# Performance work log

Hardware: AMD Instinct MI355X
Metric: run time of the kernel (lower is better)

## Reference

```python
import jax, jax.numpy as jnp
import numpy as np

VOCAB = 32000
HID = 1024
CUTOFFS = [0, 10000, 20000, 32000]
N_CLUSTERS = 2
DIV = 4
PROJ_DIMS = [HID // DIV**i for i in range(N_CLUSTERS + 1)]  # [1024, 256, 64]
# Faithful to source quirk: n_vocabs = cutoffs[i] + cutoffs[i+1]
LOGIT_DIMS = [CUTOFFS[i] + CUTOFFS[i + 1] for i in range(N_CLUSTERS + 1)]  # [10000, 30000, 52000]


def setup_inputs() -> dict:
    key = jax.random.key(0)
    ks = jax.random.split(key, 16)
    N = 2048
    inp = {
        "x": jax.random.normal(ks[0], (N, HID), dtype=jnp.float32),
        "y": jax.random.randint(ks[1], (N,), 0, VOCAB, dtype=jnp.int64),
    }
    s = 0.02
    # projections: Linear(hidden, proj_dims[i], bias=False); stored as [in, out]
    inp["Wp0"] = jax.random.normal(ks[2], (HID, PROJ_DIMS[0]), dtype=jnp.float32) * s
    inp["Wp1"] = jax.random.normal(ks[3], (HID, PROJ_DIMS[1]), dtype=jnp.float32) * s
    inp["Wp2"] = jax.random.normal(ks[4], (HID, PROJ_DIMS[2]), dtype=jnp.float32) * s
    # logits: Linear(proj_dims[i], LOGIT_DIMS[i]) with bias
    inp["Wl0"] = jax.random.normal(ks[5], (PROJ_DIMS[0], LOGIT_DIMS[0]), dtype=jnp.float32) * s
    inp["bl0"] = jnp.zeros((LOGIT_DIMS[0],), dtype=jnp.float32)
    inp["Wl1"] = jax.random.normal(ks[6], (PROJ_DIMS[1], LOGIT_DIMS[1]), dtype=jnp.float32) * s
    inp["bl1"] = jnp.zeros((LOGIT_DIMS[1],), dtype=jnp.float32)
    inp["Wl2"] = jax.random.normal(ks[7], (PROJ_DIMS[2], LOGIT_DIMS[2]), dtype=jnp.float32) * s
    inp["bl2"] = jnp.zeros((LOGIT_DIMS[2],), dtype=jnp.float32)
    # cluster_logit: Linear(hidden, n_clusters)
    inp["Wc"] = jax.random.normal(ks[8], (HID, N_CLUSTERS), dtype=jnp.float32) * s
    inp["bc"] = jnp.zeros((N_CLUSTERS,), dtype=jnp.float32)
    return inp


def reference(x, y, Wp0, Wp1, Wp2, Wl0, bl0, Wl1, bl1, Wl2, bl2, Wc, bc):
    # head: project (dim-preserving here) then head-vocab logits + cluster logits
    head_proj = x @ Wp0                                   # [N, 1024]
    head_logit = jnp.concatenate(
        [head_proj @ Wl0 + bl0, head_proj @ Wc + bc], axis=1
    )                                                     # [N, 10000 + 2]
    head_lp = jax.nn.log_softmax(head_logit, axis=1)

    nll = jnp.zeros(y.shape, dtype=x.dtype)

    # cluster 0: targets in [0, cutoffs[1])
    m0 = (y >= CUTOFFS[0]) & (y < CUTOFFS[1])
    t0 = jnp.clip(y - CUTOFFS[0], 0, head_lp.shape[1] - 1)
    lp0 = jnp.take_along_axis(head_lp, t0[:, None], axis=1)[:, 0]
    nll = jnp.where(m0, -lp0, nll)

    # tail clusters: small projection GEMM + log_softmax + gather, combined via masks
    tails = [(Wp1, Wl1, bl1), (Wp2, Wl2, bl2)]
    for i, (Wp, Wl, bl) in enumerate(tails, start=1):
        l, r = CUTOFFS[i], CUTOFFS[i + 1]
        mask = (y >= l) & (y < r)
        t = jnp.clip(y - l, 0, Wl.shape[1] - 1)
        tail_lp = jax.nn.log_softmax((x @ Wp) @ Wl + bl, axis=1)  # [N, LOGIT_DIMS[i]]
        # faithful to source: head column -i (reversed cluster order quirk)
        lp = head_lp[:, -i] + jnp.take_along_axis(tail_lp, t[:, None], axis=1)[:, 0]
        nll = jnp.where(mask, -lp, nll)

    return nll
```

## Files before the change

### kernel.cpp

```cpp
#include <hip/hip_runtime.h>
#include <math.h>

#define HID 1024
#define NROWS 2048

typedef __attribute__((ext_vector_type(8))) short short8;
typedef __attribute__((ext_vector_type(4))) short short4_t;
typedef __attribute__((ext_vector_type(4))) float f32x4;

__device__ __forceinline__ short f2bf(float f) {
  union { float f; unsigned u; } v; v.f = f;
  unsigned r = v.u + 0x7fffu + ((v.u >> 16) & 1u);
  return (short)(r >> 16);
}
__device__ __forceinline__ float bf2f(short s) {
  union { unsigned u; float f; } v; v.u = ((unsigned)(unsigned short)s) << 16;
  return v.f;
}
__device__ __forceinline__ float wave_sum(float a) {
#pragma unroll
  for (int off = 32; off; off >>= 1) a += __shfl_xor(a, off, 64);
  return a;
}

__global__ __launch_bounds__(256) void prep(
    const float* __restrict__ x, const int* __restrict__ y,
    const float* __restrict__ Wp0, const float* __restrict__ Wp1,
    const float* __restrict__ Wp2, const float* __restrict__ Wl0,
    const float* __restrict__ Wl1, const float* __restrict__ Wl2,
    short* __restrict__ xb,
    int* __restrict__ counts, int* __restrict__ slot_of_row,
    int* __restrict__ rows1, int* __restrict__ rows2,
    short* __restrict__ T0, short* __restrict__ T1, short* __restrict__ T2,
    short* __restrict__ T3, short* __restrict__ T4, short* __restrict__ T5) {
  const int tid = threadIdx.x;
  int b = blockIdx.x;
  if (b == 0) {
    __shared__ int c1s, c2s;
    if (tid == 0) { c1s = 0; c2s = 0; }
    __syncthreads();
    for (int r = tid; r < NROWS; r += 256) {
      const int yy = y[r];
      if (yy >= 20000) {
        const int s = atomicAdd(&c2s, 1);
        slot_of_row[r] = s; rows2[s] = r;
      } else if (yy >= 10000) {
        const int s = atomicAdd(&c1s, 1);
        slot_of_row[r] = s; rows1[s] = r;
      } else {
        slot_of_row[r] = -1;
      }
    }
    __syncthreads();
    if (tid == 0) { counts[0] = NROWS; counts[1] = c1s; counts[2] = c2s; }
    return;
  }
  if (b <= 2048) {
    const int i = ((b - 1) * 256 + tid) * 4;
    short4_t o;
    o.x = f2bf(x[i + 0]); o.y = f2bf(x[i + 1]);
    o.z = f2bf(x[i + 2]); o.w = f2bf(x[i + 3]);
    *(short4_t*)&xb[i] = o;
    return;
  }
  b -= 2049;
  const float* W; short* BT; int K, N, Npad, tn;
  if (b < 1024)                { W = Wp0; BT = T0; K = 1024; N = 1024;  Npad = 1024;  tn = 32;   }
  else if ((b -= 1024) < 256)  { W = Wp1; BT = T1; K = 1024; N = 256;   Npad = 256;   tn = 8;    }
  else if ((b -= 256) < 128)   { W = Wp2; BT = T2; K = 1024; N = 64;    Npad = 128;   tn = 4;    }
  else if ((b -= 128) < 10112) { W = Wl0; BT = T3; K = 1024; N = 10000; Npad = 10112; tn = 316;  }
  else if ((b -= 10112) < 7520){ W = Wl1; BT = T4; K = 256;  N = 30000; Npad = 30080; tn = 940;  }
  else { b -= 7520;              W = Wl2; BT = T5; K = 64;   N = 52000; Npad = 52096; tn = 1628; }

  __shared__ float T[32][33];
  const int n0 = (b % tn) * 32, k0 = (b / tn) * 32;
  const int r = tid >> 3, c = (tid & 7) * 4;
  float v0 = 0.f, v1 = 0.f, v2 = 0.f, v3 = 0.f;
  const float* p = &W[(size_t)(k0 + r) * N];
  if (n0 + c + 3 < N) {
    v0 = p[n0 + c]; v1 = p[n0 + c + 1]; v2 = p[n0 + c + 2]; v3 = p[n0 + c + 3];
  } else {
    if (n0 + c + 0 < N) v0 = p[n0 + c + 0];
    if (n0 + c + 1 < N) v1 = p[n0 + c + 1];
    if (n0 + c + 2 < N) v2 = p[n0 + c + 2];
  }
  T[r][c] = v0; T[r][c + 1] = v1; T[r][c + 2] = v2; T[r][c + 3] = v3;
  __syncthreads();
  const int nl = tid >> 3, kl = (tid & 7) * 4;
  const int n = n0 + nl;
  if (n < Npad) {
    short4_t o;
    o.x = (n < N) ? f2bf(T[kl + 0][nl]) : (short)0;
    o.y = (n < N) ? f2bf(T[kl + 1][nl]) : (short)0;
    o.z = (n < N) ? f2bf(T[kl + 2][nl]) : (short)0;
    o.w = (n < N) ? f2bf(T[kl + 3][nl]) : (short)0;
    *(short4_t*)&BT[(size_t)n * K + k0 + kl] = o;
  }
}

__device__ __forceinline__ void mfma_mainloop(const short* aB[4], const short* bB[4],
                                              short* As, short* Bs,
                                              f32x4 acc[4][4],
                                              int K, int w, int lane) {
  const int quad = lane >> 4, ln = lane & 15;
  const int wm = w >> 1, wn = w & 1;
  const int l7 = ln & 7;
  for (int kt = 0; kt < K; kt += 64) {
#pragma unroll
    for (int i = 0; i < 4; ++i) {
      const int row = w * 32 + i * 8;
      __builtin_amdgcn_global_load_lds(
          (const __attribute__((address_space(1))) void*)(aB[i] + kt),
          (__attribute__((address_space(3))) void*)(As + row * 64), 16, 0, 0);
      __builtin_amdgcn_global_load_lds(
          (const __attribute__((address_space(1))) void*)(bB[i] + kt),
          (__attribute__((address_space(3))) void*)(Bs + row * 64), 16, 0, 0);
    }
    __syncthreads();
#pragma unroll
    for (int ks = 0; ks < 2; ++ks) {
      const int kcs = ks * 4 + quad;
      short8 af[4], bfr[4];
#pragma unroll
      for (int mt = 0; mt < 4; ++mt) {
        const int row = wm * 64 + mt * 16 + ln;
        af[mt] = *(const short8*)(As + ((row * 8 + (kcs ^ l7)) << 3));
      }
#pragma unroll
      for (int nt = 0; nt < 4; ++nt) {
        const int rowb = wn * 64 + nt * 16 + ln;
        bfr[nt] = *(const short8*)(Bs + ((rowb * 8 + (kcs ^ l7)) << 3));
      }
#pragma unroll
      for (int mt = 0; mt < 4; ++mt)
#pragma unroll
        for (int nt = 0; nt < 4; ++nt)
          acc[mt][nt] = __builtin_amdgcn_mfma_f32_16x16x32_bf16(
              af[mt], bfr[nt], acc[mt][nt], 0, 0, 0);
    }
    __syncthreads();
  }
}


__global__ __launch_bounds__(256) void proj_all(
    const short* __restrict__ xb,
    const short* __restrict__ WpT0, const short* __restrict__ WpT1,
    const short* __restrict__ WpT2,
    short* __restrict__ P0b, short* __restrict__ P1c, short* __restrict__ P2c,
    const int* __restrict__ rows1, const int* __restrict__ rows2,
    const int* __restrict__ counts) {
  int b = blockIdx.x;
  const short* BT; short* C; int N, r0, c0, cnt;
  const int* rowlist = nullptr;
  if (b < 128) {
    BT = WpT0; C = P0b; N = 1024;
    c0 = (b & 7) * 128; r0 = (b >> 3) * 128; cnt = NROWS;
  } else if (b < 160) {
    b -= 128; BT = WpT1; C = P1c; N = 256;
    c0 = (b & 1) * 128; r0 = (b >> 1) * 128; rowlist = rows1; cnt = counts[1];
  } else {
    b -= 160; BT = WpT2; C = P2c; N = 64;
    c0 = 0; r0 = b * 128; rowlist = rows2; cnt = counts[2];
  }
  if (r0 >= cnt) return;

  __shared__ short As[128 * 64];
  __shared__ short Bs[128 * 64];
  const int tid = threadIdx.x;
  const int w = tid >> 6, lane = tid & 63;
  const int quad = lane >> 4, ln = lane & 15;
  const int wm = w >> 1, wn = w & 1;
  const int rsub = lane >> 3;
  const int kc = (lane & 7) ^ rsub;
  const int K = 1024;

  const short* aB[4]; const short* bB[4];
#pragma unroll
  for (int i = 0; i < 4; ++i) {
    const int sl = r0 + w * 32 + i * 8 + rsub;
    const int ar = rowlist ? rowlist[sl < cnt ? sl : cnt - 1] : sl;
    aB[i] = xb + (size_t)ar * K + kc * 8;
    bB[i] = BT + (size_t)(c0 + w * 32 + i * 8 + rsub) * K + kc * 8;
  }

  f32x4 acc[4][4];
  const f32x4 zero = {0.f, 0.f, 0.f, 0.f};
#pragma unroll
  for (int i = 0; i < 4; ++i)
#pragma unroll
    for (int j = 0; j < 4; ++j) acc[i][j] = zero;
  mfma_mainloop(aB, bB, As, Bs, acc, K, w, lane);
#pragma unroll
  for (int mt = 0; mt < 4; ++mt)
#pragma unroll
    for (int r = 0; r < 4; ++r) {
      const int grow = r0 + wm * 64 + mt * 16 + quad * 4 + r;
#pragma unroll
      for (int nt = 0; nt < 4; ++nt) {
        const int cg = c0 + wn * 64 + nt * 16 + ln;
        if (cg < N) C[(size_t)grow * N + cg] = f2bf(acc[mt][nt][r]);
      }
    }
}

#define HB  (16 * 79)
#define T1B (16 * 235)
#define T2B (16 * 407)

__global__ __launch_bounds__(256) void logit_all(
    const short* __restrict__ P0b, const short* __restrict__ WlT0,
    const float* __restrict__ bl0, float* __restrict__ psh,
    const short* __restrict__ P1c, const short* __restrict__ WlT1,
    const float* __restrict__ bl1, float* __restrict__ ps1,
    const short* __restrict__ P2c, const short* __restrict__ WlT2,
    const float* __restrict__ bl2, float* __restrict__ ps2,
    const int* __restrict__ counts) {
  int b = blockIdx.x;
  const short* A; const short* BT; const float* bias; float* ps;
  int K, Ncols, nsplit, rb, cs, cnt;
  if (b < HB) {
    A = P0b; BT = WlT0; bias = bl0; ps = psh;
    K = 1024; Ncols = 10000; nsplit = 79; rb = b / 79; cs = b % 79; cnt = NROWS;
  } else if ((b -= HB) < T1B) {
    A = P1c; BT = WlT1; bias = bl1; ps = ps1;
    K = 256; Ncols = 30000; nsplit = 235; rb = b / 235; cs = b % 235; cnt = counts[1];
  } else {
    b -= T1B;
    A = P2c; BT = WlT2; bias = bl2; ps = ps2;
    K = 64; Ncols = 52000; nsplit = 407; rb = b / 407; cs = b % 407; cnt = counts[2];
  }
  const int r0 = rb * 128, c0 = cs * 128;
  if (r0 >= cnt) return;

  __shared__ short As[128 * 64];
  __shared__ short Bs[128 * 64];
  __shared__ float psL[2][128];
  const int tid = threadIdx.x;
  const int w = tid >> 6, lane = tid & 63;
  const int quad = lane >> 4, ln = lane & 15;
  const int wm = w >> 1, wn = w & 1;
  const int rsub = lane >> 3;
  const int kc = (lane & 7) ^ rsub;

  const short* aB[4]; const short* bB[4];
#pragma unroll
  for (int i = 0; i < 4; ++i) {
    aB[i] = A + (size_t)(r0 + w * 32 + i * 8 + rsub) * K + kc * 8;
    bB[i] = BT + (size_t)(c0 + w * 32 + i * 8 + rsub) * K + kc * 8;
  }

  f32x4 acc[4][4];
  const f32x4 zero = {0.f, 0.f, 0.f, 0.f};
#pragma unroll
  for (int i = 0; i < 4; ++i)
#pragma unroll
    for (int j = 0; j < 4; ++j) acc[i][j] = zero;
  mfma_mainloop(aB, bB, As, Bs, acc, K, w, lane);

  float bv[4], vm[4];
#pragma unroll
  for (int nt = 0; nt < 4; ++nt) {
    const int cg = c0 + wn * 64 + nt * 16 + ln;
    vm[nt] = (cg < Ncols) ? 1.f : 0.f;
    bv[nt] = (cg < Ncols) ? bias[cg] : 0.f;
  }
#pragma unroll
  for (int mt = 0; mt < 4; ++mt)
#pragma unroll
    for (int r = 0; r < 4; ++r) {
      float s = 0.f;
#pragma unroll
      for (int nt = 0; nt < 4; ++nt)
        s += vm[nt] * __expf(acc[mt][nt][r] + bv[nt]);
#pragma unroll
      for (int off = 1; off < 16; off <<= 1) s += __shfl_xor(s, off, 64);
      if (ln == 0) psL[wn][wm * 64 + mt * 16 + quad * 4 + r] = s;
    }
  __syncthreads();
  if (tid < 128)
    ps[(size_t)(r0 + tid) * nsplit + cs] = psL[0][tid] + psL[1][tid];
}

__global__ __launch_bounds__(256) void finalize(
    const short* __restrict__ P0b, const short* __restrict__ P1c,
    const short* __restrict__ P2c,
    const short* __restrict__ WlT0, const float* __restrict__ bl0,
    const short* __restrict__ WlT1, const float* __restrict__ bl1,
    const short* __restrict__ WlT2, const float* __restrict__ bl2,
    const float* __restrict__ Wc, const float* __restrict__ bc,
    const int* __restrict__ y, const int* __restrict__ slot_of_row,
    const float* __restrict__ psh, const float* __restrict__ ps1,
    const float* __restrict__ ps2, float* __restrict__ out) {
  const int lane = threadIdx.x & 63;
  const int row = blockIdx.x * 4 + (threadIdx.x >> 6);

  float a0 = 0.f, a1 = 0.f;
  for (int k = lane; k < HID; k += 64) {
    const float p = bf2f(P0b[(size_t)row * HID + k]);
    a0 += p * Wc[2 * k];
    a1 += p * Wc[2 * k + 1];
  }
  a0 = wave_sum(a0);
  a1 = wave_sum(a1);
  const float cl0 = a0 + bc[0], cl1 = a1 + bc[1];

  float S = 0.f;
  for (int i = lane; i < 79; i += 64) S += psh[(size_t)row * 79 + i];
  S = wave_sum(S) + __expf(cl0) + __expf(cl1);
  const float lse = logf(S);

  const int yy = y[row];
  float nll;
  if (yy < 10000) {
    const short* pr = P0b + (size_t)row * 1024;
    const short* wr = WlT0 + (size_t)yy * 1024;
    float a = 0.f;
    for (int kk = lane * 4; kk < 1024; kk += 256) {
      const short4_t p = *(const short4_t*)(pr + kk);
      const short4_t wv = *(const short4_t*)(wr + kk);
      a += bf2f(p.x) * bf2f(wv.x) + bf2f(p.y) * bf2f(wv.y)
         + bf2f(p.z) * bf2f(wv.z) + bf2f(p.w) * bf2f(wv.w);
    }
    a = wave_sum(a);
    nll = -((a + bl0[yy]) - lse);
  } else if (yy < 20000) {
    const int t = yy - 10000;
    const int slot = slot_of_row[row];
    float S1 = 0.f;
    for (int i = lane; i < 235; i += 64) S1 += ps1[(size_t)slot * 235 + i];
    S1 = wave_sum(S1);
    const short* pr = P1c + (size_t)slot * 256;
    const short* wr = WlT1 + (size_t)t * 256;
    const int kk = lane * 4;
    const short4_t p = *(const short4_t*)(pr + kk);
    const short4_t wv = *(const short4_t*)(wr + kk);
    float a = bf2f(p.x) * bf2f(wv.x) + bf2f(p.y) * bf2f(wv.y)
            + bf2f(p.z) * bf2f(wv.z) + bf2f(p.w) * bf2f(wv.w);
    a = wave_sum(a);
    nll = -((cl1 - lse) + ((a + bl1[t]) - logf(S1)));
  } else {
    const int t = yy - 20000;
    const int slot = slot_of_row[row];
    float S2 = 0.f;
    for (int i = lane; i < 407; i += 64) S2 += ps2[(size_t)slot * 407 + i];
    S2 = wave_sum(S2);
    float a = 0.f;
    if (lane < 16) {
      const short* pr = P2c + (size_t)slot * 64;
      const short* wr = WlT2 + (size_t)t * 64;
      const int kk = lane * 4;
      const short4_t p = *(const short4_t*)(pr + kk);
      const short4_t wv = *(const short4_t*)(wr + kk);
      a = bf2f(p.x) * bf2f(wv.x) + bf2f(p.y) * bf2f(wv.y)
        + bf2f(p.z) * bf2f(wv.z) + bf2f(p.w) * bf2f(wv.w);
    }
    a = wave_sum(a);
    nll = -((cl0 - lse) + ((a + bl2[t]) - logf(S2)));
  }
  if (lane == 0) out[row] = nll;
}

extern "C" void kernel_launch(void* const* d_in, const int* in_sizes, int n_in,
                              void* d_out, int out_size, void* d_ws, size_t ws_size,
                              hipStream_t stream) {
  const float* x   = (const float*)d_in[0];
  const int*   y   = (const int*)d_in[1];
  const float* Wp0 = (const float*)d_in[2];
  const float* Wp1 = (const float*)d_in[3];
  const float* Wp2 = (const float*)d_in[4];
  const float* Wl0 = (const float*)d_in[5];
  const float* bl0 = (const float*)d_in[6];
  const float* Wl1 = (const float*)d_in[7];
  const float* bl1 = (const float*)d_in[8];
  const float* Wl2 = (const float*)d_in[9];
  const float* bl2 = (const float*)d_in[10];
  const float* Wc  = (const float*)d_in[11];
  const float* bc  = (const float*)d_in[12];
  float* out = (float*)d_out;

  float* fws = (float*)d_ws;
  float* psh = fws; fws += (size_t)NROWS * 79;
  float* ps1 = fws; fws += (size_t)NROWS * 235;
  float* ps2 = fws; fws += (size_t)NROWS * 407;
  int* iws = (int*)fws;
  int* counts      = iws; iws += 4;
  int* slot_of_row = iws; iws += NROWS;
  int* rows1       = iws; iws += NROWS;
  int* rows2       = iws; iws += NROWS;
  short* sp = (short*)iws;
  short* xb   = sp; sp += (size_t)NROWS * 1024;
  short* P0b  = sp; sp += (size_t)NROWS * 1024;
  short* P1c  = sp; sp += (size_t)NROWS * 256;
  short* P2c  = sp; sp += (size_t)NROWS * 64;
  short* WpT0 = sp; sp += (size_t)1024 * 1024;
  short* WpT1 = sp; sp += (size_t)256 * 1024;
  short* WpT2 = sp; sp += (size_t)128 * 1024;
  short* WlT0 = sp; sp += (size_t)10112 * 1024;
  short* WlT1 = sp; sp += (size_t)30080 * 256;
  short* WlT2 = sp; sp += (size_t)52096 * 64;

  dim3 blk(256);
  prep<<<dim3(24345), blk, 0, stream>>>(x, y, Wp0, Wp1, Wp2, Wl0, Wl1, Wl2,
                                        xb, counts, slot_of_row, rows1, rows2,
                                        WpT0, WpT1, WpT2, WlT0, WlT1, WlT2);
  proj_all<<<dim3(176), blk, 0, stream>>>(xb, WpT0, WpT1, WpT2, P0b, P1c, P2c,
                                          rows1, rows2, counts);
  logit_all<<<dim3(HB + T1B + T2B), blk, 0, stream>>>(
      P0b, WlT0, bl0, psh, P1c, WlT1, bl1, ps1, P2c, WlT2, bl2, ps2, counts);
  finalize<<<dim3(NROWS / 4), blk, 0, stream>>>(
      P0b, P1c, P2c, WlT0, bl0, WlT1, bl1, WlT2, bl2, Wc, bc, y, slot_of_row,
      psh, ps1, ps2, out);
}
```

Measured before the change: 318.9 us.

## Overlap logit weight transposes with projection GEMM; persistent XCD-aware logit kernel

```diff
diff --git a/kernel.cpp b/kernel.cpp
--- a/kernel.cpp
+++ b/kernel.cpp
@@ -23,16 +23,44 @@
   return a;
 }
 
-__global__ __launch_bounds__(256) void prep(
+__device__ __forceinline__ void transpose_tile(const float* __restrict__ W,
+                                               short* __restrict__ BT,
+                                               int K, int N, int Npad, int tn,
+                                               int b, int tid) {
+  __shared__ float T[32][33];
+  const int n0 = (b % tn) * 32, k0 = (b / tn) * 32;
+  const int r = tid >> 3, c = (tid & 7) * 4;
+  float v0 = 0.f, v1 = 0.f, v2 = 0.f, v3 = 0.f;
+  const float* p = &W[(size_t)(k0 + r) * N];
+  if (n0 + c + 3 < N) {
+    v0 = p[n0 + c]; v1 = p[n0 + c + 1]; v2 = p[n0 + c + 2]; v3 = p[n0 + c + 3];
+  } else {
+    if (n0 + c + 0 < N) v0 = p[n0 + c + 0];
+    if (n0 + c + 1 < N) v1 = p[n0 + c + 1];
+    if (n0 + c + 2 < N) v2 = p[n0 + c + 2];
+  }
+  T[r][c] = v0; T[r][c + 1] = v1; T[r][c + 2] = v2; T[r][c + 3] = v3;
+  __syncthreads();
+  const int nl = tid >> 3, kl = (tid & 7) * 4;
+  const int n = n0 + nl;
+  if (n < Npad) {
+    short4_t o;
+    o.x = (n < N) ? f2bf(T[kl + 0][nl]) : (short)0;
+    o.y = (n < N) ? f2bf(T[kl + 1][nl]) : (short)0;
+    o.z = (n < N) ? f2bf(T[kl + 2][nl]) : (short)0;
+    o.w = (n < N) ? f2bf(T[kl + 3][nl]) : (short)0;
+    *(short4_t*)&BT[(size_t)n * K + k0 + kl] = o;
+  }
+}
+
+__global__ __launch_bounds__(256) void prep1(
     const float* __restrict__ x, const int* __restrict__ y,
     const float* __restrict__ Wp0, const float* __restrict__ Wp1,
-    const float* __restrict__ Wp2, const float* __restrict__ Wl0,
-    const float* __restrict__ Wl1, const float* __restrict__ Wl2,
+    const float* __restrict__ Wp2,
     short* __restrict__ xb,
     int* __restrict__ counts, int* __restrict__ slot_of_row,
     int* __restrict__ rows1, int* __restrict__ rows2,
-    short* __restrict__ T0, short* __restrict__ T1, short* __restrict__ T2,
-    short* __restrict__ T3, short* __restrict__ T4, short* __restrict__ T5) {
+    short* __restrict__ T0, short* __restrict__ T1, short* __restrict__ T2) {
   const int tid = threadIdx.x;
   int b = blockIdx.x;
   if (b == 0) {
@@ -64,38 +92,9 @@
     return;
   }
   b -= 2049;
-  const float* W; short* BT; int K, N, Npad, tn;
-  if (b < 1024)                { W = Wp0; BT = T0; K = 1024; N = 1024;  Npad = 1024;  tn = 32;   }
-  else if ((b -= 1024) < 256)  { W = Wp1; BT = T1; K = 1024; N = 256;   Npad = 256;   tn = 8;    }
-  else if ((b -= 256) < 128)   { W = Wp2; BT = T2; K = 1024; N = 64;    Npad = 128;   tn = 4;    }
-  else if ((b -= 128) < 10112) { W = Wl0; BT = T3; K = 1024; N = 10000; Npad = 10112; tn = 316;  }
-  else if ((b -= 10112) < 7520){ W = Wl1; BT = T4; K = 256;  N = 30000; Npad = 30080; tn = 940;  }
-  else { b -= 7520;              W = Wl2; BT = T5; K = 64;   N = 52000; Npad = 52096; tn = 1628; }
-
-  __shared__ float T[32][33];
-  const int n0 = (b % tn) * 32, k0 = (b / tn) * 32;
-  const int r = tid >> 3, c = (tid & 7) * 4;
-  float v0 = 0.f, v1 = 0.f, v2 = 0.f, v3 = 0.f;
-  const float* p = &W[(size_t)(k0 + r) * N];
-  if (n0 + c + 3 < N) {
-    v0 = p[n0 + c]; v1 = p[n0 + c + 1]; v2 = p[n0 + c + 2]; v3 = p[n0 + c + 3];
-  } else {
-    if (n0 + c + 0 < N) v0 = p[n0 + c + 0];
-    if (n0 + c + 1 < N) v1 = p[n0 + c + 1];
-    if (n0 + c + 2 < N) v2 = p[n0 + c + 2];
-  }
-  T[r][c] = v0; T[r][c + 1] = v1; T[r][c + 2] = v2; T[r][c + 3] = v3;
-  __syncthreads();
-  const int nl = tid >> 3, kl = (tid & 7) * 4;
-  const int n = n0 + nl;
-  if (n < Npad) {
-    short4_t o;
-    o.x = (n < N) ? f2bf(T[kl + 0][nl]) : (short)0;
-    o.y = (n < N) ? f2bf(T[kl + 1][nl]) : (short)0;
-    o.z = (n < N) ? f2bf(T[kl + 2][nl]) : (short)0;
-    o.w = (n < N) ? f2bf(T[kl + 3][nl]) : (short)0;
-    *(short4_t*)&BT[(size_t)n * K + k0 + kl] = o;
-  }
+  if (b < 1024)               transpose_tile(Wp0, T0, 1024, 1024, 1024, 32, b, tid);
+  else if ((b -= 1024) < 256) transpose_tile(Wp1, T1, 1024, 256, 256, 8, b, tid);
+  else { b -= 256;            transpose_tile(Wp2, T2, 1024, 64, 128, 4, b, tid); }
 }
 
 __device__ __forceinline__ void mfma_mainloop(const short* aB[4], const short* bB[4],
@@ -143,14 +142,26 @@
 }
 
 
-__global__ __launch_bounds__(256) void proj_all(
+__global__ __launch_bounds__(256) void launch2(
     const short* __restrict__ xb,
     const short* __restrict__ WpT0, const short* __restrict__ WpT1,
     const short* __restrict__ WpT2,
     short* __restrict__ P0b, short* __restrict__ P1c, short* __restrict__ P2c,
     const int* __restrict__ rows1, const int* __restrict__ rows2,
-    const int* __restrict__ counts) {
+    const int* __restrict__ counts,
+    const float* __restrict__ Wl0, const float* __restrict__ Wl1,
+    const float* __restrict__ Wl2,
+    short* __restrict__ WlT0, short* __restrict__ WlT1,
+    short* __restrict__ WlT2) {
   int b = blockIdx.x;
+  const int tid = threadIdx.x;
+  if (b >= 176) {
+    b -= 176;
+    if (b < 10112)               transpose_tile(Wl0, WlT0, 1024, 10000, 10112, 316, b, tid);
+    else if ((b -= 10112) < 7520) transpose_tile(Wl1, WlT1, 256, 30000, 30080, 940, b, tid);
+    else { b -= 7520;             transpose_tile(Wl2, WlT2, 64, 52000, 52096, 1628, b, tid); }
+    return;
+  }
   const short* BT; short* C; int N, r0, c0, cnt;
   const int* rowlist = nullptr;
   if (b < 128) {
@@ -167,7 +178,6 @@
 
   __shared__ short As[128 * 64];
   __shared__ short Bs[128 * 64];
-  const int tid = threadIdx.x;
   const int w = tid >> 6, lane = tid & 63;
   const int quad = lane >> 4, ln = lane & 15;
   const int wm = w >> 1, wn = w & 1;
@@ -204,11 +214,7 @@
     }
 }
 
-#define HB  (16 * 79)
-#define T1B (16 * 235)
-#define T2B (16 * 407)
-
-__global__ __launch_bounds__(256) void logit_all(
+__global__ __launch_bounds__(256, 5) void logit_persist(
     const short* __restrict__ P0b, const short* __restrict__ WlT0,
     const float* __restrict__ bl0, float* __restrict__ psh,
     const short* __restrict__ P1c, const short* __restrict__ WlT1,
@@ -216,26 +222,9 @@
     const short* __restrict__ P2c, const short* __restrict__ WlT2,
     const float* __restrict__ bl2, float* __restrict__ ps2,
     const int* __restrict__ counts) {
-  int b = blockIdx.x;
-  const short* A; const short* BT; const float* bias; float* ps;
-  int K, Ncols, nsplit, rb, cs, cnt;
-  if (b < HB) {
-    A = P0b; BT = WlT0; bias = bl0; ps = psh;
-    K = 1024; Ncols = 10000; nsplit = 79; rb = b / 79; cs = b % 79; cnt = NROWS;
-  } else if ((b -= HB) < T1B) {
-    A = P1c; BT = WlT1; bias = bl1; ps = ps1;
-    K = 256; Ncols = 30000; nsplit = 235; rb = b / 235; cs = b % 235; cnt = counts[1];
-  } else {
-    b -= T1B;
-    A = P2c; BT = WlT2; bias = bl2; ps = ps2;
-    K = 64; Ncols = 52000; nsplit = 407; rb = b / 407; cs = b % 407; cnt = counts[2];
-  }
-  const int r0 = rb * 128, c0 = cs * 128;
-  if (r0 >= cnt) return;
-
   __shared__ short As[128 * 64];
   __shared__ short Bs[128 * 64];
-  __shared__ float psL[2][128];
+  float* psL = (float*)As;
   const int tid = threadIdx.x;
   const int w = tid >> 6, lane = tid & 63;
   const int quad = lane >> 4, ln = lane & 15;
@@ -243,43 +232,74 @@
   const int rsub = lane >> 3;
   const int kc = (lane & 7) ^ rsub;
 
-  const short* aB[4]; const short* bB[4];
-#pragma unroll
-  for (int i = 0; i < 4; ++i) {
-    aB[i] = A + (size_t)(r0 + w * 32 + i * 8 + rsub) * K + kc * 8;
-    bB[i] = BT + (size_t)(c0 + w * 32 + i * 8 + rsub) * K + kc * 8;
-  }
-
-  f32x4 acc[4][4];
-  const f32x4 zero = {0.f, 0.f, 0.f, 0.f};
-#pragma unroll
-  for (int i = 0; i < 4; ++i)
-#pragma unroll
-    for (int j = 0; j < 4; ++j) acc[i][j] = zero;
-  mfma_mainloop(aB, bB, As, Bs, acc, K, w, lane);
-
-  float bv[4], vm[4];
-#pragma unroll
-  for (int nt = 0; nt < 4; ++nt) {
-    const int cg = c0 + wn * 64 + nt * 16 + ln;
-    vm[nt] = (cg < Ncols) ? 1.f : 0.f;
-    bv[nt] = (cg < Ncols) ? bias[cg] : 0.f;
-  }
-#pragma unroll
-  for (int mt = 0; mt < 4; ++mt)
-#pragma unroll
-    for (int r = 0; r < 4; ++r) {
-      float s = 0.f;
-#pragma unroll
-      for (int nt = 0; nt < 4; ++nt)
-        s += vm[nt] * __expf(acc[mt][nt][r] + bv[nt]);
-#pragma unroll
-      for (int off = 1; off < 16; off <<= 1) s += __shfl_xor(s, off, 64);
-      if (ln == 0) psL[wn][wm * 64 + mt * 16 + quad * 4 + r] = s;
-    }
-  __syncthreads();
-  if (tid < 128)
-    ps[(size_t)(r0 + tid) * nsplit + cs] = psL[0][tid] + psL[1][tid];
+  const int xcd = blockIdx.x & 7;
+  const int lid = blockIdx.x >> 3;
+  const int nrb1 = (counts[1] + 127) >> 7;
+  const int nrb2 = (counts[2] + 127) >> 7;
+  const int nch = (xcd < 7) ? 10 : 9;
+  const int nc1 = (xcd < 7) ? 30 : 25;
+  const int nc2 = (xcd < 7) ? 51 : 50;
+  const int nh = nch * 16, n1 = nc1 * nrb1, n2 = nc2 * nrb2;
+  const int T = nh + n1 + n2;
+
+  for (int t = lid; t < T; t += 160) {
+    const short* A; const short* BT; const float* bias; float* ps;
+    int K, Ncols, nsplit, rb, cs;
+    int tt = t;
+    if (tt < nh) {
+      rb = tt / nch; cs = xcd * 10 + tt % nch;
+      A = P0b; BT = WlT0; bias = bl0; ps = psh;
+      K = 1024; Ncols = 10000; nsplit = 79;
+    } else if ((tt -= nh) < n1) {
+      cs = xcd * 30 + tt / nrb1; rb = tt % nrb1;
+      A = P1c; BT = WlT1; bias = bl1; ps = ps1;
+      K = 256; Ncols = 30000; nsplit = 235;
+    } else {
+      tt -= n1;
+      cs = xcd * 51 + tt / nrb2; rb = tt % nrb2;
+      A = P2c; BT = WlT2; bias = bl2; ps = ps2;
+      K = 64; Ncols = 52000; nsplit = 407;
+    }
+    const int r0 = rb * 128, c0 = cs * 128;
+
+    const short* aB[4]; const short* bB[4];
+#pragma unroll
+    for (int i = 0; i < 4; ++i) {
+      aB[i] = A + (size_t)(r0 + w * 32 + i * 8 + rsub) * K + kc * 8;
+      bB[i] = BT + (size_t)(c0 + w * 32 + i * 8 + rsub) * K + kc * 8;
+    }
+
+    f32x4 acc[4][4];
+    const f32x4 zero = {0.f, 0.f, 0.f, 0.f};
+#pragma unroll
+    for (int i = 0; i < 4; ++i)
+#pragma unroll
+      for (int j = 0; j < 4; ++j) acc[i][j] = zero;
+    __syncthreads();
+    mfma_mainloop(aB, bB, As, Bs, acc, K, w, lane);
+
+    float bv[4];
+#pragma unroll
+    for (int nt = 0; nt < 4; ++nt) {
+      const int cg = c0 + wn * 64 + nt * 16 + ln;
+      bv[nt] = (cg < Ncols) ? bias[cg] : -1.0e30f;
+    }
+#pragma unroll
+    for (int mt = 0; mt < 4; ++mt)
+#pragma unroll
+      for (int r = 0; r < 4; ++r) {
+        float s = 0.f;
+#pragma unroll
+        for (int nt = 0; nt < 4; ++nt)
+          s += __expf(acc[mt][nt][r] + bv[nt]);
+#pragma unroll
+        for (int off = 1; off < 16; off <<= 1) s += __shfl_xor(s, off, 64);
+        if (ln == 0) psL[wn * 128 + wm * 64 + mt * 16 + quad * 4 + r] = s;
+      }
+    __syncthreads();
+    if (tid < 128)
+      ps[(size_t)(r0 + tid) * nsplit + cs] = psL[tid] + psL[128 + tid];
+  }
 }
 
 __global__ __launch_bounds__(256) void finalize(
@@ -401,12 +421,13 @@
   short* WlT2 = sp; sp += (size_t)52096 * 64;
 
   dim3 blk(256);
-  prep<<<dim3(24345), blk, 0, stream>>>(x, y, Wp0, Wp1, Wp2, Wl0, Wl1, Wl2,
-                                        xb, counts, slot_of_row, rows1, rows2,
-                                        WpT0, WpT1, WpT2, WlT0, WlT1, WlT2);
-  proj_all<<<dim3(176), blk, 0, stream>>>(xb, WpT0, WpT1, WpT2, P0b, P1c, P2c,
-                                          rows1, rows2, counts);
-  logit_all<<<dim3(HB + T1B + T2B), blk, 0, stream>>>(
+  prep1<<<dim3(3457), blk, 0, stream>>>(x, y, Wp0, Wp1, Wp2, xb,
+                                        counts, slot_of_row, rows1, rows2,
+                                        WpT0, WpT1, WpT2);
+  launch2<<<dim3(21064), blk, 0, stream>>>(xb, WpT0, WpT1, WpT2,
+                                           P0b, P1c, P2c, rows1, rows2, counts,
+                                           Wl0, Wl1, Wl2, WlT0, WlT1, WlT2);
+  logit_persist<<<dim3(1280), blk, 0, stream>>>(
       P0b, WlT0, bl0, psh, P1c, WlT1, bl1, ps1, P2c, WlT2, bl2, ps2, counts);
   finalize<<<dim3(NROWS / 4), blk, 0, stream>>>(
       P0b, P1c, P2c, WlT0, bl0, WlT1, bl1, WlT2, bl2, Wc, bc, y, slot_of_row,
```

Result: slower. 427.8 us (+34.2%).
